# Performance work log

Measured on AMD Instinct MI355X. Metric: run time of the kernel, lower is better.

The kernel has to match this reference:

```python
import jax, jax.numpy as jnp
import numpy as np
import math

DIM, HEADS = 512, 8
D_K = DIM // HEADS

def setup_inputs() -> dict:
    key = jax.random.key(0)
    ks = jax.random.split(key, 6)
    B, LK, LQ = 16, 2048, 256
    s = 1.0 / math.sqrt(DIM)
    return {
        "L": jax.random.normal(ks[0], (B, LK, DIM), jnp.float32),
        "G": jax.random.normal(ks[1], (B, LQ, DIM), jnp.float32),
        "Wq": jax.random.normal(ks[2], (DIM, DIM), jnp.float32) * s,
        "bq": jnp.zeros((DIM,), jnp.float32),
        "Wo": jax.random.normal(ks[3], (DIM, DIM), jnp.float32) * s,
        "bo": jnp.zeros((DIM,), jnp.float32),
    }

def reference(L, G, Wq, bq, Wo, bo):
    B = G.shape[0]
    # Q projection from global tokens; K,V are raw local features split into heads
    q = (G @ Wq + bq).reshape(B, -1, HEADS, D_K)          # [B, Lq, H, d]
    k = L.reshape(B, -1, HEADS, D_K)                      # [B, Lk, H, d]
    v = k
    # double scaling as in source: / sqrt(d_k) * dim**-0.5
    scale = (D_K ** -0.5) * (DIM ** -0.5)
    dots = jnp.einsum("bqhd,bkhd->bhqk", q, k) * scale    # [B, H, Lq, Lk]
    attn = jax.nn.softmax(dots, axis=-1)
    x = jnp.einsum("bhqk,bkhd->bqhd", attn, v)            # [B, Lq, H, d]
    x = x.reshape(B, -1, HEADS * D_K)
    return x @ Wo + bo
```

## Files before the change

### kernel.cpp

```cpp
#include <hip/hip_runtime.h>

#define KSTR 72

typedef __attribute__((ext_vector_type(8))) short short8;
typedef __attribute__((ext_vector_type(4))) float f32x4;

#define EXP2F(x) __builtin_amdgcn_exp2f(x)

__device__ __forceinline__ unsigned short f2bf(float f) {
    union { float f; unsigned u; } v; v.f = f;
    unsigned r = v.u + 0x7fff + ((v.u >> 16) & 1);
    return (unsigned short)(r >> 16);
}
__device__ __forceinline__ unsigned pk2(float a, float b) {
    return (unsigned)f2bf(a) | ((unsigned)f2bf(b) << 16);
}

__global__ __launch_bounds__(256) void conv_W(const float* __restrict__ Wq,
                                              const float* __restrict__ Wo,
                                              unsigned short* __restrict__ WqF,
                                              unsigned short* __restrict__ WoF) {
    const float* W = blockIdx.y ? Wo : Wq;
    unsigned short* WF = blockIdx.y ? WoF : WqF;
    int g = blockIdx.x * 256 + threadIdx.x;
    int lane = g & 63, ntg = (g >> 6) & 31, kt = g >> 11;
    int c = lane & 15, quad = lane >> 4;
    const float* wp = W + (size_t)(32 * kt + 8 * quad) * 512 + 16 * ntg + c;
    float v[8];
    #pragma unroll
    for (int j = 0; j < 8; j++) v[j] = wp[(size_t)j * 512];
    uint4 u;
    u.x = pk2(v[0], v[1]); u.y = pk2(v[2], v[3]);
    u.z = pk2(v[4], v[5]); u.w = pk2(v[6], v[7]);
    *(uint4*)(WF + (size_t)g * 8) = u;
}

__global__ __launch_bounds__(256) void conv_L(const float* __restrict__ Lmat,
                                              unsigned short* __restrict__ KF,
                                              unsigned short* __restrict__ VF) {
    __shared__ unsigned short KFs[4096];
    __shared__ unsigned short VFs[4096];
    const int blk = blockIdx.x;
    const int t = blk & 31, h = (blk >> 5) & 7, b = blk >> 8;
    const int tid = threadIdx.x;
    const int key = tid & 63, wv = tid >> 6;

    const float* src = Lmat + ((size_t)(b * 2048 + 64 * t + key)) * 512 + 64 * h + 16 * wv;
    float4 a0 = *(const float4*)src;
    float4 a1 = *(const float4*)(src + 4);
    float4 a2 = *(const float4*)(src + 8);
    float4 a3 = *(const float4*)(src + 12);
    float vals[16] = {a0.x, a0.y, a0.z, a0.w, a1.x, a1.y, a1.z, a1.w,
                      a2.x, a2.y, a2.z, a2.w, a3.x, a3.y, a3.z, a3.w};
    #pragma unroll
    for (int i = 0; i < 16; i++) {
        int d = 16 * wv + i;
        unsigned short bv = f2bf(vals[i]);
        KFs[((((key >> 4) * 2 + (d >> 5)) * 64) + ((d >> 3) & 3) * 16 + (key & 15)) * 8 + (d & 7)] = bv;
        VFs[((((d >> 4) * 2 + (key >> 5)) * 64) + ((key >> 3) & 3) * 16 + (d & 15)) * 8 + (key & 7)] = bv;
    }
    __syncthreads();
    size_t gbase = (size_t)blk * 4096 + tid * 16;
    *(uint4*)(KF + gbase)     = *(const uint4*)&KFs[tid * 16];
    *(uint4*)(KF + gbase + 8) = *(const uint4*)&KFs[tid * 16 + 8];
    *(uint4*)(VF + gbase)     = *(const uint4*)&VFs[tid * 16];
    *(uint4*)(VF + gbase + 8) = *(const uint4*)&VFs[tid * 16 + 8];
}

template<bool A_BF16, bool OUT_BF16>
__global__ __launch_bounds__(256, 2) void gemm_direct(const void* __restrict__ Ap,
                                                      const unsigned short* __restrict__ WF,
                                                      const float* __restrict__ bias,
                                                      void* __restrict__ Cp,
                                                      float oscale) {
    const int tid = threadIdx.x;
    const int wv = tid >> 6, lane = tid & 63;
    const int c = lane & 15, quad = lane >> 4;
    const int m0 = blockIdx.x * 64, n0 = blockIdx.y * 64;
    const int row = m0 + 16 * wv + c;

    f32x4 acc[4];
    #pragma unroll
    for (int nt = 0; nt < 4; nt++) acc[nt] = (f32x4){0.f, 0.f, 0.f, 0.f};

    #pragma unroll
    for (int kk = 0; kk < 16; kk++) {
        short8 af;
        if (A_BF16) {
            af = *(const short8*)((const unsigned short*)Ap + (size_t)row * 512 + 32 * kk + 8 * quad);
        } else {
            const float* ap = (const float*)Ap + (size_t)row * 512 + 32 * kk + 8 * quad;
            float4 x0 = *(const float4*)ap;
            float4 x1 = *(const float4*)(ap + 4);
            af[0] = (short)f2bf(x0.x); af[1] = (short)f2bf(x0.y);
            af[2] = (short)f2bf(x0.z); af[3] = (short)f2bf(x0.w);
            af[4] = (short)f2bf(x1.x); af[5] = (short)f2bf(x1.y);
            af[6] = (short)f2bf(x1.z); af[7] = (short)f2bf(x1.w);
        }
        #pragma unroll
        for (int nt = 0; nt < 4; nt++) {
            short8 bf = *(const short8*)(WF +
                (((size_t)kk * 32 + (n0 >> 4) + nt) * 64 + lane) * 8);
            acc[nt] = __builtin_amdgcn_mfma_f32_16x16x32_bf16(af, bf, acc[nt], 0, 0, 0);
        }
    }

    #pragma unroll
    for (int nt = 0; nt < 4; nt++) {
        float bv = bias[n0 + 16 * nt + c];
        #pragma unroll
        for (int r = 0; r < 4; r++) {
            float v = (acc[nt][r] + bv) * oscale;
            size_t idx = (size_t)(m0 + 16 * wv + 4 * quad + r) * 512 + n0 + 16 * nt + c;
            if (OUT_BF16) ((unsigned short*)Cp)[idx] = f2bf(v);
            else          ((float*)Cp)[idx] = v;
        }
    }
}

#define GLD(dst, base, off) \
    asm volatile("global_load_dwordx4 %0, %1, off offset:" #off \
                 : "=v"(dst) : "v"(base) : "memory")
#define WAITV(n) asm volatile("s_waitcnt vmcnt(" #n ")" ::: "memory")
#define SCHEDB() __builtin_amdgcn_sched_barrier(0)

__global__ __launch_bounds__(256, 2) void attn_frag(const unsigned short* __restrict__ Q,
                                                    const unsigned short* __restrict__ KF,
                                                    const unsigned short* __restrict__ VF,
                                                    unsigned short* __restrict__ X) {
    __shared__ unsigned short Pw[4][16 * KSTR];

    const int raw = blockIdx.x;
    const int h  = raw & 7;
    const int qt = (raw >> 3) & 3;
    const int b  = raw >> 5;
    const int tid = threadIdx.x;
    const int wv = tid >> 6, lane = tid & 63;
    const int c = lane & 15, quad = lane >> 4;

    short8 qa[2];
    {
        const unsigned short* qsrc =
            Q + ((size_t)(b * 256 + qt * 64 + 16 * wv + c)) * 512 + h * 64;
        qa[0] = *(const short8*)(qsrc + 8 * quad);
        qa[1] = *(const short8*)(qsrc + 32 + 8 * quad);
    }
    WAITV(0); SCHEDB();

    short8 ones;
    #pragma unroll
    for (int i = 0; i < 8; i++) ones[i] = (short)0x3F80;

    f32x4 oacc[4];
    #pragma unroll
    for (int dt = 0; dt < 4; dt++) oacc[dt] = (f32x4){0.f, 0.f, 0.f, 0.f};
    f32x4 lacc = (f32x4){0.f, 0.f, 0.f, 0.f};

    const int swc = (c >> 3) & 1;
    const int swr = (quad >> 1) & 1;

    const unsigned short* kf = KF + ((size_t)((b * 8 + h) * 32)) * 4096 + lane * 8;
    const unsigned short* vf = VF + ((size_t)((b * 8 + h) * 32)) * 4096 + lane * 8;

    short8 kc[8], vc[8], kn[8], vn[8];

#define ISSUE_TILE(kb, vb, tp) do { \
        const unsigned short* k2_ = kf + (size_t)(tp) * 4096; \
        const unsigned short* v2_ = vf + (size_t)(tp) * 4096; \
        const unsigned short* k3_ = k2_ + 2048; \
        const unsigned short* v3_ = v2_ + 2048; \
        GLD(kb[0], k2_, 0);    GLD(kb[1], k2_, 1024); \
        GLD(kb[2], k2_, 2048); GLD(kb[3], k2_, 3072); \
        GLD(kb[4], k3_, 0);    GLD(kb[5], k3_, 1024); \
        GLD(kb[6], k3_, 2048); GLD(kb[7], k3_, 3072); \
        GLD(vb[0], v2_, 0);    GLD(vb[1], v2_, 1024); \
        GLD(vb[2], v2_, 2048); GLD(vb[3], v2_, 3072); \
        GLD(vb[4], v3_, 0);    GLD(vb[5], v3_, 1024); \
        GLD(vb[6], v3_, 2048); GLD(vb[7], v3_, 3072); \
    } while (0)

    auto compute = [&](short8* kb, short8* vb) {
        f32x4 sacc[4];
        #pragma unroll
        for (int nt = 0; nt < 4; nt++) sacc[nt] = (f32x4){0.f, 0.f, 0.f, 0.f};
        #pragma unroll
        for (int nt = 0; nt < 4; nt++)
            #pragma unroll
            for (int ks = 0; ks < 2; ks++)
                sacc[nt] = __builtin_amdgcn_mfma_f32_16x16x32_bf16(
                    qa[ks], kb[nt * 2 + ks], sacc[nt], 0, 0, 0);
        #pragma unroll
        for (int nt = 0; nt < 4; nt++)
            #pragma unroll
            for (int r = 0; r < 4; r++)
                Pw[wv][(4 * quad + r) * KSTR + ((16 * nt + c) ^ (8 * swr))] =
                    f2bf(EXP2F(sacc[nt][r]));
        short8 pa0 = *(const short8*)&Pw[wv][c * KSTR + (8 * (quad ^ swc))];
        short8 pa1 = *(const short8*)&Pw[wv][c * KSTR + 32 + (8 * (quad ^ swc))];
        #pragma unroll
        for (int dt = 0; dt < 4; dt++) {
            oacc[dt] = __builtin_amdgcn_mfma_f32_16x16x32_bf16(pa0, vb[dt * 2], oacc[dt], 0, 0, 0);
            oacc[dt] = __builtin_amdgcn_mfma_f32_16x16x32_bf16(pa1, vb[dt * 2 + 1], oacc[dt], 0, 0, 0);
        }
        lacc = __builtin_amdgcn_mfma_f32_16x16x32_bf16(pa0, ones, lacc, 0, 0, 0);
        lacc = __builtin_amdgcn_mfma_f32_16x16x32_bf16(pa1, ones, lacc, 0, 0, 0);
    };

    ISSUE_TILE(kc, vc, 0);
    for (int t = 0; t < 32; t += 2) {
        ISSUE_TILE(kn, vn, t + 1);
        WAITV(16); SCHEDB();
        compute(kc, vc);
        if (t + 2 < 32) {
            ISSUE_TILE(kc, vc, t + 2);
            WAITV(16); SCHEDB();
        } else {
            WAITV(0); SCHEDB();
        }
        compute(kn, vn);
    }

    #pragma unroll
    for (int r = 0; r < 4; r++) {
        float inv = 1.f / lacc[r];
        size_t row = (size_t)(b * 256 + qt * 64 + 16 * wv + 4 * quad + r);
        unsigned short* xp = X + row * 512 + h * 64;
        #pragma unroll
        for (int dt = 0; dt < 4; dt++)
            xp[16 * dt + c] = f2bf(oacc[dt][r] * inv);
    }
#undef ISSUE_TILE
}

extern "C" void kernel_launch(void* const* d_in, const int* in_sizes, int n_in,
                              void* d_out, int out_size, void* d_ws, size_t ws_size,
                              hipStream_t stream) {
    const float* Lmat = (const float*)d_in[0];
    const float* G    = (const float*)d_in[1];
    const float* Wq   = (const float*)d_in[2];
    const float* bq   = (const float*)d_in[3];
    const float* Wo   = (const float*)d_in[4];
    const float* bo   = (const float*)d_in[5];
    float* out = (float*)d_out;

    const float SCe = 0.005524271728019903f * 1.4426950408889634f;
    dim3 gg(64, 8);

    unsigned short* Qws = (unsigned short*)d_ws;
    unsigned short* Xws = Qws + (size_t)2097152;
    unsigned short* WqF = Xws + (size_t)2097152;
    unsigned short* WoF = WqF + (size_t)262144;
    unsigned short* KF  = WoF + (size_t)262144;
    unsigned short* VF  = KF  + (size_t)16777216;

    conv_W<<<dim3(128, 2), 256, 0, stream>>>(Wq, Wo, WqF, WoF);
    conv_L<<<4096, 256, 0, stream>>>(Lmat, KF, VF);
    gemm_direct<false, true><<<gg, 256, 0, stream>>>(G, WqF, bq, Qws, SCe);
    attn_frag<<<512, 256, 0, stream>>>(Qws, KF, VF, Xws);
    gemm_direct<true, false><<<gg, 256, 0, stream>>>(Xws, WoF, bo, out, 1.0f);
}
```

Before: 179.9 us.

## Software-pipeline QK of next tile with softmax/PV of current tile

Restructures the attention loop so the QK MFMA for tile t+1 is issued before the PV MFMA for tile t, with P double-buffered in shared memory and K/V loads split and staggered. This lets the exp and LDS round-trip of one tile overlap with matrix work of the next, instead of serialising QK, exp, store and PV. It also raises wave priority around MFMA blocks with s_setprio. The cost is extra registers for a second score accumulator, double the LDS per wave, and more delicate vmcnt accounting.

New measurement: 180.6 us. Within noise of the previous version (+0.4%).

```diff
diff --git a/kernel.cpp b/kernel.cpp
--- a/kernel.cpp
+++ b/kernel.cpp
@@ -128,7 +128,7 @@
                                                     const unsigned short* __restrict__ KF,
                                                     const unsigned short* __restrict__ VF,
                                                     unsigned short* __restrict__ X) {
-    __shared__ unsigned short Pw[4][16 * KSTR];
+    __shared__ unsigned short Pw[4][2][16 * KSTR];
 
     const int raw = blockIdx.x;
     const int h  = raw & 7;
@@ -163,40 +163,41 @@
     const unsigned short* vf = VF + ((size_t)((b * 8 + h) * 32)) * 4096 + lane * 8;
 
     short8 kc[8], vc[8], kn[8], vn[8];
-
-#define ISSUE_TILE(kb, vb, tp) do { \
-        const unsigned short* k2_ = kf + (size_t)(tp) * 4096; \
-        const unsigned short* v2_ = vf + (size_t)(tp) * 4096; \
-        const unsigned short* k3_ = k2_ + 2048; \
-        const unsigned short* v3_ = v2_ + 2048; \
-        GLD(kb[0], k2_, 0);    GLD(kb[1], k2_, 1024); \
-        GLD(kb[2], k2_, 2048); GLD(kb[3], k2_, 3072); \
-        GLD(kb[4], k3_, 0);    GLD(kb[5], k3_, 1024); \
-        GLD(kb[6], k3_, 2048); GLD(kb[7], k3_, 3072); \
-        GLD(vb[0], v2_, 0);    GLD(vb[1], v2_, 1024); \
-        GLD(vb[2], v2_, 2048); GLD(vb[3], v2_, 3072); \
-        GLD(vb[4], v3_, 0);    GLD(vb[5], v3_, 1024); \
-        GLD(vb[6], v3_, 2048); GLD(vb[7], v3_, 3072); \
+    f32x4 sA[4], sB[4];
+
+#define ISSUE8(buf, bp, tp) do { \
+        const unsigned short* p2_ = (bp) + (size_t)(tp) * 4096; \
+        const unsigned short* p3_ = p2_ + 2048; \
+        GLD(buf[0], p2_, 0);    GLD(buf[1], p2_, 1024); \
+        GLD(buf[2], p2_, 2048); GLD(buf[3], p2_, 3072); \
+        GLD(buf[4], p3_, 0);    GLD(buf[5], p3_, 1024); \
+        GLD(buf[6], p3_, 2048); GLD(buf[7], p3_, 3072); \
     } while (0)
 
-    auto compute = [&](short8* kb, short8* vb) {
-        f32x4 sacc[4];
-        #pragma unroll
-        for (int nt = 0; nt < 4; nt++) sacc[nt] = (f32x4){0.f, 0.f, 0.f, 0.f};
+    auto qk = [&](f32x4* S, short8* kb) {
+        #pragma unroll
+        for (int nt = 0; nt < 4; nt++) S[nt] = (f32x4){0.f, 0.f, 0.f, 0.f};
+        __builtin_amdgcn_s_setprio(1);
         #pragma unroll
         for (int nt = 0; nt < 4; nt++)
             #pragma unroll
             for (int ks = 0; ks < 2; ks++)
-                sacc[nt] = __builtin_amdgcn_mfma_f32_16x16x32_bf16(
-                    qa[ks], kb[nt * 2 + ks], sacc[nt], 0, 0, 0);
+                S[nt] = __builtin_amdgcn_mfma_f32_16x16x32_bf16(
+                    qa[ks], kb[nt * 2 + ks], S[nt], 0, 0, 0);
+        __builtin_amdgcn_s_setprio(0);
+    };
+    auto store_p = [&](f32x4* S, int buf) {
         #pragma unroll
         for (int nt = 0; nt < 4; nt++)
             #pragma unroll
             for (int r = 0; r < 4; r++)
-                Pw[wv][(4 * quad + r) * KSTR + ((16 * nt + c) ^ (8 * swr))] =
-                    f2bf(EXP2F(sacc[nt][r]));
-        short8 pa0 = *(const short8*)&Pw[wv][c * KSTR + (8 * (quad ^ swc))];
-        short8 pa1 = *(const short8*)&Pw[wv][c * KSTR + 32 + (8 * (quad ^ swc))];
+                Pw[wv][buf][(4 * quad + r) * KSTR + ((16 * nt + c) ^ (8 * swr))] =
+                    f2bf(EXP2F(S[nt][r]));
+    };
+    auto pv = [&](short8* vb, int buf) {
+        short8 pa0 = *(const short8*)&Pw[wv][buf][c * KSTR + (8 * (quad ^ swc))];
+        short8 pa1 = *(const short8*)&Pw[wv][buf][c * KSTR + 32 + (8 * (quad ^ swc))];
+        __builtin_amdgcn_s_setprio(1);
         #pragma unroll
         for (int dt = 0; dt < 4; dt++) {
             oacc[dt] = __builtin_amdgcn_mfma_f32_16x16x32_bf16(pa0, vb[dt * 2], oacc[dt], 0, 0, 0);
@@ -204,20 +205,32 @@
         }
         lacc = __builtin_amdgcn_mfma_f32_16x16x32_bf16(pa0, ones, lacc, 0, 0, 0);
         lacc = __builtin_amdgcn_mfma_f32_16x16x32_bf16(pa1, ones, lacc, 0, 0, 0);
-    };
-
-    ISSUE_TILE(kc, vc, 0);
-    for (int t = 0; t < 32; t += 2) {
-        ISSUE_TILE(kn, vn, t + 1);
-        WAITV(16); SCHEDB();
-        compute(kc, vc);
-        if (t + 2 < 32) {
-            ISSUE_TILE(kc, vc, t + 2);
-            WAITV(16); SCHEDB();
+        __builtin_amdgcn_s_setprio(0);
+    };
+
+    auto body = [&](int t, f32x4* scur, f32x4* snext, short8* knext,
+                    short8* vcur, short8* vnext, short8* kiss) {
+        if (t + 1 < 32) ISSUE8(vnext, vf, t + 1);
+        store_p(scur, t & 1);
+        if (t + 1 < 32) {
+            WAITV(8); SCHEDB();
+            qk(snext, knext);
         } else {
             WAITV(0); SCHEDB();
         }
-        compute(kn, vn);
+        pv(vcur, t & 1);
+        if (t + 2 < 32) ISSUE8(kiss, kf, t + 2);
+    };
+
+    ISSUE8(kc, kf, 0);
+    ISSUE8(vc, vf, 0);
+    ISSUE8(kn, kf, 1);
+    WAITV(16); SCHEDB();
+    qk(sA, kc);
+
+    for (int t = 0; t < 32; t += 2) {
+        body(t,     sA, sB, kn, vc, vn, kc);
+        body(t + 1, sB, sA, kc, vn, vc, kn);
     }
 
     #pragma unroll
@@ -229,7 +242,7 @@
         for (int dt = 0; dt < 4; dt++)
             xp[16 * dt + c] = f2bf(oacc[dt][r] * inv);
     }
-#undef ISSUE_TILE
+#undef ISSUE8
 }
 
 extern "C" void kernel_launch(void* const* d_in, const int* in_sizes, int n_in,
```
